# Optimization experiments

Hardware: AMD Instinct MI355X
Metric: run time of the kernel (lower is better)

Reference implementation:

```python
import jax, jax.numpy as jnp
import numpy as np

N_NODES = 50000
K_EIG = 512
F_DIM = 128


def setup_inputs() -> dict:
    key = jax.random.key(0)
    k1, k2, k3 = jax.random.split(key, 3)
    eigenvectors = jax.random.normal(k1, (N_NODES, K_EIG), dtype=jnp.float32)
    spectral_filters = jax.random.normal(k2, (K_EIG,), dtype=jnp.float32)
    x = jax.random.normal(k3, (N_NODES, F_DIM), dtype=jnp.float32)
    return {"eigenvectors": eigenvectors, "spectral_filters": spectral_filters, "x": x}


def reference(eigenvectors, spectral_filters, x):
    # U @ diag(g) @ U.T @ x  ==  U @ (g[:, None] * (U.T @ x)); relu epilogue.
    spec = eigenvectors.T @ x                      # [k, f]
    logits = eigenvectors @ (spectral_filters[:, None] * spec)  # [n, f]
    return jax.nn.relu(logits)
```

## Files before the change

### kernel.cpp

```cpp
#include <hip/hip_runtime.h>
#include <hip/hip_bf16.h>

#define N_NODES 50000
#define K_EIG   512
#define F_DIM   128
#define NPAD    51200
#define NSPLITS 160
#define CHUNK   320
#define NT32    1600
#define NT16    3200

typedef __attribute__((ext_vector_type(8))) short bf16x8;
typedef __attribute__((ext_vector_type(4))) short s16x4;
typedef __attribute__((ext_vector_type(4))) float f32x4;
typedef __attribute__((ext_vector_type(2))) unsigned u32x2;

static __device__ __forceinline__ unsigned pk2(float lo, float hi) {
    unsigned short a = __builtin_bit_cast(unsigned short, __float2bfloat16(lo));
    unsigned short b = __builtin_bit_cast(unsigned short, __float2bfloat16(hi));
    return ((unsigned)b << 16) | (unsigned)a;
}

static __device__ __forceinline__ short f2bf(float f) {
    union { float f; unsigned u; } v; v.f = f;
    unsigned r = v.u + 0x7fffu + ((v.u >> 16) & 1u);
    return (short)(r >> 16);
}

static __device__ __forceinline__ float bf2f(unsigned short u) {
    union { unsigned u; float f; } v; v.u = ((unsigned)u) << 16;
    return v.f;
}

__global__ __launch_bounds__(256) void prep_x(const float* __restrict__ x,
                                              unsigned short* __restrict__ xTa)
{
    const int n0 = blockIdx.x * 64;
    const int f0 = blockIdx.y * 64;
    const int fa = threadIdx.x & 15;
    const int nb = threadIdx.x >> 4;
    const int n  = n0 + 4 * nb;
    const int f  = f0 + 4 * fa;

    float r[4][4];
    #pragma unroll
    for (int jj = 0; jj < 4; ++jj) {
        int nr = n + jj;
        if (nr < N_NODES) {
            f32x4 v = *reinterpret_cast<const f32x4*>(x + (long)nr * F_DIM + f);
            r[jj][0] = v[0]; r[jj][1] = v[1]; r[jj][2] = v[2]; r[jj][3] = v[3];
        } else {
            r[jj][0] = r[jj][1] = r[jj][2] = r[jj][3] = 0.f;
        }
    }
    const int nt32 = n >> 5;
    const int hpart = ((n >> 3) & 3) * 16;
    const int slot  = 4 * (nb & 1);
    #pragma unroll
    for (int i = 0; i < 4; ++i) {
        int fi = f + i;
        size_t ad = ((size_t)((fi >> 4) * NT32 + nt32) * 64 + hpart + (fi & 15)) * 8 + slot;
        u32x2 w; w[0] = pk2(r[0][i], r[1][i]); w[1] = pk2(r[2][i], r[3][i]);
        *reinterpret_cast<u32x2*>(xTa + ad) = w;
    }
}

__global__ __launch_bounds__(256) void prep_u(const float* __restrict__ U,
                                              unsigned short* __restrict__ UTa,
                                              unsigned short* __restrict__ Ubfa)
{
    __shared__ unsigned char lds1[64 * 128];
    __shared__ unsigned char lds2[64 * 128];

    const int n0  = blockIdx.x * 64;
    const int k0  = blockIdx.y * 64;
    const int tid = threadIdx.x;
    const int kq  = tid & 15;
    const int nq  = tid >> 4;

    float r[4][4];
    #pragma unroll
    for (int j = 0; j < 4; ++j) {
        int n = n0 + 4 * nq + j;
        if (n < N_NODES) {
            f32x4 v = *reinterpret_cast<const f32x4*>(U + (long)n * K_EIG + k0 + 4 * kq);
            r[j][0] = v[0]; r[j][1] = v[1]; r[j][2] = v[2]; r[j][3] = v[3];
        } else {
            r[j][0] = r[j][1] = r[j][2] = r[j][3] = 0.f;
        }
    }

    #pragma unroll
    for (int i = 0; i < 4; ++i) {
        int kl = 4 * kq + i;
        unsigned lo = pk2(r[0][i], r[1][i]);
        unsigned hi = pk2(r[2][i], r[3][i]);
        int byte = (kl * 128 + 8 * nq) ^ ((kl & 7) << 4);
        *reinterpret_cast<unsigned long long*>(lds1 + byte) =
            ((unsigned long long)hi << 32) | (unsigned long long)lo;
    }
    #pragma unroll
    for (int j = 0; j < 4; ++j) {
        int nl = 4 * nq + j;
        unsigned lo = pk2(r[j][0], r[j][1]);
        unsigned hi = pk2(r[j][2], r[j][3]);
        int byte = (nl * 128 + 8 * kq) ^ ((nl & 7) << 4);
        *reinterpret_cast<unsigned long long*>(lds2 + byte) =
            ((unsigned long long)hi << 32) | (unsigned long long)lo;
    }
    __syncthreads();

    const int q = tid & 31;
    {
        const int fid = tid >> 5;
        const int ntl = fid >> 1;
        const int ktl = fid & 1;
        #pragma unroll
        for (int e = 0; e < 2; ++e) {
            int l    = 2 * q + e;
            int row  = ntl * 16 + (l & 15);
            int byte = (row * 128 + ktl * 64 + 16 * (l >> 4)) ^ ((row & 7) << 4);
            bf16x8 v = *reinterpret_cast<const bf16x8*>(lds2 + byte);
            size_t ad = (((size_t)(n0 >> 4) + ntl) * 16 + ((k0 >> 5) + ktl)) * 64 + l;
            *reinterpret_cast<bf16x8*>(Ubfa + ad * 8) = v;
        }
    }
    {
        const int fid = tid >> 5;
        const int ktl = fid >> 1;
        const int ntl = fid & 1;
        #pragma unroll
        for (int e = 0; e < 2; ++e) {
            int l    = 2 * q + e;
            int row  = ktl * 16 + (l & 15);
            int byte = (row * 128 + ntl * 64 + 16 * (l >> 4)) ^ ((row & 7) << 4);
            bf16x8 v = *reinterpret_cast<const bf16x8*>(lds1 + byte);
            size_t ad = (((size_t)(k0 >> 4) + ktl) * NT32 + ((n0 >> 5) + ntl)) * 64 + l;
            *reinterpret_cast<bf16x8*>(UTa + ad * 8) = v;
        }
    }
}

__global__ __launch_bounds__(256) void k_spec(
    const unsigned short* __restrict__ UTa, const unsigned short* __restrict__ xTa,
    unsigned short* __restrict__ part2)
{
    const int ktB   = blockIdx.x;
    const int split = blockIdx.y;
    const int tid   = threadIdx.x;
    const int wid   = tid >> 6;
    const int lane  = tid & 63;
    const int nt0   = split * (CHUNK / 32);

    f32x4 acc[4][2];
    #pragma unroll
    for (int s = 0; s < 4; ++s)
        #pragma unroll
        for (int t = 0; t < 2; ++t)
            #pragma unroll
            for (int e = 0; e < 4; ++e) acc[s][t][e] = 0.f;

    const unsigned short* Abase = UTa + ((size_t)(ktB * 4) * NT32) * 512 + lane * 8;
    const unsigned short* Bbase = xTa + ((size_t)(wid * 2) * NT32) * 512 + lane * 8;

    bf16x8 aC[4], bC[2];
    #pragma unroll
    for (int s = 0; s < 4; ++s)
        aC[s] = *reinterpret_cast<const bf16x8*>(Abase + ((size_t)s * NT32 + nt0) * 512);
    #pragma unroll
    for (int t = 0; t < 2; ++t)
        bC[t] = *reinterpret_cast<const bf16x8*>(Bbase + ((size_t)t * NT32 + nt0) * 512);

    for (int step = 0; step < CHUNK / 32; ++step) {
        int ntn = nt0 + ((step + 1 < CHUNK / 32) ? step + 1 : 0);
        bf16x8 aN[4], bN[2];
        #pragma unroll
        for (int s = 0; s < 4; ++s)
            aN[s] = *reinterpret_cast<const bf16x8*>(Abase + ((size_t)s * NT32 + ntn) * 512);
        #pragma unroll
        for (int t = 0; t < 2; ++t)
            bN[t] = *reinterpret_cast<const bf16x8*>(Bbase + ((size_t)t * NT32 + ntn) * 512);

        #pragma unroll
        for (int s = 0; s < 4; ++s)
            #pragma unroll
            for (int t = 0; t < 2; ++t)
                acc[s][t] = __builtin_amdgcn_mfma_f32_16x16x32_bf16(
                    aC[s], bC[t], acc[s][t], 0, 0, 0);

        #pragma unroll
        for (int s = 0; s < 4; ++s) aC[s] = aN[s];
        #pragma unroll
        for (int t = 0; t < 2; ++t) bC[t] = bN[t];
    }

    unsigned short* pb = part2 + (((size_t)(ktB * NSPLITS + split)) * 256 + tid) * 32;
    #pragma unroll
    for (int s = 0; s < 4; ++s) {
        bf16x8 v;
        #pragma unroll
        for (int e = 0; e < 4; ++e) {
            v[e]     = f2bf(acc[s][0][e]);
            v[e + 4] = f2bf(acc[s][1][e]);
        }
        *reinterpret_cast<bf16x8*>(pb + s * 8) = v;
    }
}

__global__ __launch_bounds__(256) void k_reduce1(
    const unsigned short* __restrict__ part2, float* __restrict__ part3)
{
    const int q  = blockIdx.x * 256 + threadIdx.x;
    const int pg = blockIdx.y;
    const int kt = q >> 11;
    const int tp = (q >> 3) & 255;
    const int sl = q & 7;
    f32x4 s; s[0] = s[1] = s[2] = s[3] = 0.f;
    const int pend = pg * 20 + 20;
    for (int p = pg * 20; p < pend; ++p) {
        s16x4 v = *reinterpret_cast<const s16x4*>(
            part2 + (((size_t)(kt * NSPLITS + p)) * 256 + tp) * 32 + sl * 4);
        s[0] += bf2f((unsigned short)v[0]); s[1] += bf2f((unsigned short)v[1]);
        s[2] += bf2f((unsigned short)v[2]); s[3] += bf2f((unsigned short)v[3]);
    }
    *reinterpret_cast<f32x4*>(part3 + ((size_t)pg * 16384 + q) * 4) = s;
}

__global__ __launch_bounds__(256) void k_reduce2(
    const float* __restrict__ part3, const float* __restrict__ g,
    unsigned short* __restrict__ specbfa)
{
    const int q = blockIdx.x * 256 + threadIdx.x;
    f32x4 s; s[0] = s[1] = s[2] = s[3] = 0.f;
    #pragma unroll
    for (int pg = 0; pg < 8; ++pg) {
        f32x4 v = *reinterpret_cast<const f32x4*>(part3 + ((size_t)pg * 16384 + q) * 4);
        s[0] += v[0]; s[1] += v[1]; s[2] += v[2]; s[3] += v[3];
    }
    const int kt = q >> 11, tp = (q >> 3) & 255, sl = q & 7;
    const int wid = tp >> 6, le = tp & 63, hh = le >> 4, mm = le & 15;
    const int ss = sl >> 1, tt = sl & 1;
    const int f = wid * 32 + tt * 16 + mm;
    const int k = kt * 64 + ss * 16 + hh * 4;
    f32x4 gv = *reinterpret_cast<const f32x4*>(g + k);
    s16x4 o;
    #pragma unroll
    for (int e = 0; e < 4; ++e) o[e] = f2bf(s[e] * gv[e]);
    const int lanep = ((k >> 3) & 3) * 16 + (f & 15);
    size_t ad = ((size_t)((f >> 4) * 16 + (k >> 5)) * 64 + lanep) * 8 + (k & 7);
    *reinterpret_cast<s16x4*>(specbfa + ad) = o;
}

__global__ __launch_bounds__(256) void k_out_bf(
    const unsigned short* __restrict__ Ubfa,
    const unsigned short* __restrict__ specbfa,
    float* __restrict__ out)
{
    const int tid  = threadIdx.x;
    const int wid  = tid >> 6;
    const int lane = tid & 63;
    const int h = lane >> 4, m = lane & 15;
    const int wr = wid >> 1, wc = wid & 1;
    const int nbase = blockIdx.x * 64 + wr * 32;
    const int fbase = wc * 64;

    const unsigned short* Al[2];
    #pragma unroll
    for (int i = 0; i < 2; ++i)
        Al[i] = Ubfa + ((size_t)((nbase >> 4) + i) * 8192 + lane * 8);
    const unsigned short* Blp[4];
    #pragma unroll
    for (int t = 0; t < 4; ++t)
        Blp[t] = specbfa + ((size_t)(4 * wc + t) * 8192 + lane * 8);

    f32x4 acc[2][4];
    #pragma unroll
    for (int i = 0; i < 2; ++i)
        #pragma unroll
        for (int t = 0; t < 4; ++t)
            #pragma unroll
            for (int e = 0; e < 4; ++e) acc[i][t][e] = 0.f;

    bf16x8 aC[2], bC[4];
    #pragma unroll
    for (int i = 0; i < 2; ++i) aC[i] = *reinterpret_cast<const bf16x8*>(Al[i]);
    #pragma unroll
    for (int t = 0; t < 4; ++t) bC[t] = *reinterpret_cast<const bf16x8*>(Blp[t]);

    for (int kb = 0; kb < 16; ++kb) {
        int kn = (kb + 1 < 16) ? kb + 1 : 0;
        bf16x8 aN[2], bN[4];
        #pragma unroll
        for (int i = 0; i < 2; ++i)
            aN[i] = *reinterpret_cast<const bf16x8*>(Al[i] + (size_t)kn * 512);
        #pragma unroll
        for (int t = 0; t < 4; ++t)
            bN[t] = *reinterpret_cast<const bf16x8*>(Blp[t] + (size_t)kn * 512);

        #pragma unroll
        for (int i = 0; i < 2; ++i)
            #pragma unroll
            for (int t = 0; t < 4; ++t)
                acc[i][t] = __builtin_amdgcn_mfma_f32_16x16x32_bf16(
                    aC[i], bC[t], acc[i][t], 0, 0, 0);

        #pragma unroll
        for (int i = 0; i < 2; ++i) aC[i] = aN[i];
        #pragma unroll
        for (int t = 0; t < 4; ++t) bC[t] = bN[t];
    }

    #pragma unroll
    for (int i = 0; i < 2; ++i)
        #pragma unroll
        for (int r = 0; r < 4; ++r) {
            int nn = nbase + 16 * i + 4 * h + r;
            if (nn < N_NODES) {
                float* orow = out + (long)nn * F_DIM + fbase + m;
                #pragma unroll
                for (int t = 0; t < 4; ++t)
                    orow[16 * t] = fmaxf(acc[i][t][r], 0.f);
            }
        }
}

__global__ __launch_bounds__(256) void k_spec_v1(
    const float* __restrict__ U, const float* __restrict__ g,
    const float* __restrict__ x, float* __restrict__ specT)
{
    const int kt    = blockIdx.x;
    const int split = blockIdx.y;
    const int tid   = threadIdx.x;
    const int wid   = tid >> 6;
    const int lane  = tid & 63;
    const int h     = lane >> 4;
    const int m     = lane & 15;
    const int k0 = kt * 64;
    const int f0 = wid * 32;
    const int chunk1 = 782;
    const int n_start = split * chunk1;
    int n_end = n_start + chunk1;
    if (n_end > N_NODES) n_end = N_NODES;

    f32x4 acc[4][2];
    #pragma unroll
    for (int s = 0; s < 4; ++s)
        #pragma unroll
        for (int t = 0; t < 2; ++t)
            #pragma unroll
            for (int e = 0; e < 4; ++e) acc[s][t][e] = 0.f;

    for (int nb = n_start; nb < n_end; nb += 32) {
        bf16x8 a[4]; bf16x8 b[2];
        const int nrow = nb + 8 * h;
        #pragma unroll
        for (int j = 0; j < 8; ++j) {
            int nn = nrow + j;
            bool valid = (nn < n_end);
            int nc = valid ? nn : (n_end - 1);
            const float* Urow = U + (long)nc * K_EIG + k0 + m;
            const float* Xrow = x + (long)nc * F_DIM + f0 + m;
            #pragma unroll
            for (int s = 0; s < 4; ++s) {
                short bv = f2bf(Urow[16 * s]);
                a[s][j] = valid ? bv : (short)0;
            }
            #pragma unroll
            for (int t = 0; t < 2; ++t) {
                short bv = f2bf(Xrow[16 * t]);
                b[t][j] = valid ? bv : (short)0;
            }
        }
        #pragma unroll
        for (int s = 0; s < 4; ++s)
            #pragma unroll
            for (int t = 0; t < 2; ++t)
                acc[s][t] = __builtin_amdgcn_mfma_f32_16x16x32_bf16(
                    a[s], b[t], acc[s][t], 0, 0, 0);
    }
    #pragma unroll
    for (int s = 0; s < 4; ++s)
        #pragma unroll
        for (int t = 0; t < 2; ++t)
            #pragma unroll
            for (int r = 0; r < 4; ++r) {
                int k = k0 + 16 * s + 4 * h + r;
                int f = f0 + 16 * t + m;
                atomicAdd(&specT[(long)f * K_EIG + k], acc[s][t][r] * g[k]);
            }
}

__global__ __launch_bounds__(256) void k_out_v1(
    const float* __restrict__ U, const float* __restrict__ specT,
    float* __restrict__ out)
{
    const int tid  = threadIdx.x;
    const int wid  = tid >> 6;
    const int lane = tid & 63;
    const int h = lane >> 4, m = lane & 15;
    const int wr = wid >> 1, wc = wid & 1;
    const int nbase = blockIdx.x * 128 + wr * 64;
    const int fbase = wc * 64;

    f32x4 acc[4][4];
    #pragma unroll
    for (int i = 0; i < 4; ++i)
        #pragma unroll
        for (int t = 0; t < 4; ++t)
            #pragma unroll
            for (int e = 0; e < 4; ++e) acc[i][t][e] = 0.f;

    for (int kb = 0; kb < K_EIG; kb += 32) {
        bf16x8 a[4], b[4];
        #pragma unroll
        for (int i = 0; i < 4; ++i) {
            int nn = nbase + 16 * i + m;
            bool valid = (nn < N_NODES);
            int nc = valid ? nn : (N_NODES - 1);
            const f32x4* p = reinterpret_cast<const f32x4*>(
                U + (long)nc * K_EIG + kb + 8 * h);
            f32x4 lo = p[0], hi = p[1];
            #pragma unroll
            for (int j = 0; j < 4; ++j) {
                short b0 = f2bf(lo[j]), b1 = f2bf(hi[j]);
                a[i][j]     = valid ? b0 : (short)0;
                a[i][j + 4] = valid ? b1 : (short)0;
            }
        }
        #pragma unroll
        for (int t = 0; t < 4; ++t) {
            const f32x4* p = reinterpret_cast<const f32x4*>(
                specT + (long)(fbase + 16 * t + m) * K_EIG + kb + 8 * h);
            f32x4 lo = p[0], hi = p[1];
            #pragma unroll
            for (int j = 0; j < 4; ++j) {
                b[t][j]     = f2bf(lo[j]);
                b[t][j + 4] = f2bf(hi[j]);
            }
        }
        #pragma unroll
        for (int i = 0; i < 4; ++i)
            #pragma unroll
            for (int t = 0; t < 4; ++t)
                acc[i][t] = __builtin_amdgcn_mfma_f32_16x16x32_bf16(
                    a[i], b[t], acc[i][t], 0, 0, 0);
    }
    #pragma unroll
    for (int i = 0; i < 4; ++i)
        #pragma unroll
        for (int r = 0; r < 4; ++r) {
            int nn = nbase + 16 * i + 4 * h + r;
            if (nn < N_NODES) {
                float* orow = out + (long)nn * F_DIM + fbase + m;
                #pragma unroll
                for (int t = 0; t < 4; ++t)
                    orow[16 * t] = fmaxf(acc[i][t][r], 0.f);
            }
        }
}

extern "C" void kernel_launch(void* const* d_in, const int* in_sizes, int n_in,
                              void* d_out, int out_size, void* d_ws, size_t ws_size,
                              hipStream_t stream) {
    const float* U = (const float*)d_in[0];
    const float* g = (const float*)d_in[1];
    const float* x = (const float*)d_in[2];
    float* out = (float*)d_out;

    const size_t OFF_XTA   = 0;
    const size_t OFF_UTA   = 13107200;
    const size_t OFF_UBFA  = 65536000;
    const size_t OFF_PART2 = 117964800;
    const size_t OFF_PART3 = 138936320;
    const size_t OFF_SPECA = 141033472;
    const size_t WS_NEEDED = 141164544;

    if (ws_size >= WS_NEEDED) {
        unsigned short* xTa     = (unsigned short*)((char*)d_ws + OFF_XTA);
        unsigned short* UTa     = (unsigned short*)((char*)d_ws + OFF_UTA);
        unsigned short* Ubfa    = (unsigned short*)((char*)d_ws + OFF_UBFA);
        unsigned short* part2   = (unsigned short*)((char*)d_ws + OFF_PART2);
        float*          part3   = (float*)((char*)d_ws + OFF_PART3);
        unsigned short* specbfa = (unsigned short*)((char*)d_ws + OFF_SPECA);

        dim3 gx(NPAD / 64, F_DIM / 64);
        prep_x<<<gx, 256, 0, stream>>>(x, xTa);

        dim3 gu(NPAD / 64, K_EIG / 64);
        prep_u<<<gu, 256, 0, stream>>>(U, UTa, Ubfa);

        dim3 g1(K_EIG / 64, NSPLITS);
        k_spec<<<g1, 256, 0, stream>>>(UTa, xTa, part2);

        dim3 gr1(64, 8);
        k_reduce1<<<gr1, 256, 0, stream>>>(part2, part3);
        k_reduce2<<<64, 256, 0, stream>>>(part3, g, specbfa);

        int nb2 = (N_NODES + 63) / 64;
        k_out_bf<<<nb2, 256, 0, stream>>>(Ubfa, specbfa, out);
    } else {
        float* specT = (float*)d_ws;
        hipMemsetAsync(specT, 0, (size_t)K_EIG * F_DIM * sizeof(float), stream);
        dim3 g1(K_EIG / 64, 64);
        k_spec_v1<<<g1, 256, 0, stream>>>(U, g, x, specT);
        int nb2 = (N_NODES + 127) / 128;
        k_out_v1<<<nb2, 256, 0, stream>>>(U, specT, out);
    }
}
```

Measured before the change: 107.1 us.

## Process four node tiles per prep_u block with register prefetch and double-buffered LDS

The prep_u conversion kernel now handles four consecutive 64-node tiles per block instead of one, shrinking the grid fourfold. While the current tile is packed and transposed through LDS, it loads the next tile's fp32 values into registers, and it alternates between two LDS buffers so only one barrier per tile is needed. The aim is to hide global load latency and cut block launch overhead in this bandwidth-bound prep step. The cost is more registers and LDS per block and less parallelism across the grid.

```diff
diff --git a/kernel.cpp b/kernel.cpp
--- a/kernel.cpp
+++ b/kernel.cpp
@@ -69,19 +69,25 @@
                                               unsigned short* __restrict__ UTa,
                                               unsigned short* __restrict__ Ubfa)
 {
-    __shared__ unsigned char lds1[64 * 128];
-    __shared__ unsigned char lds2[64 * 128];
-
-    const int n0  = blockIdx.x * 64;
+    __shared__ unsigned char lds1[2][64 * 128];
+    __shared__ unsigned char lds2[2][64 * 128];
+
+    const int ng  = blockIdx.x * 256;
     const int k0  = blockIdx.y * 64;
     const int tid = threadIdx.x;
     const int kq  = tid & 15;
     const int nq  = tid >> 4;
 
-    float r[4][4];
+    const int fid = tid >> 5;
+    const int q   = tid & 31;
+    const int ntlU = fid >> 1, ktlU = fid & 1;
+    const int ktlT = fid >> 1, ntlT = fid & 1;
+
+    float r[4][4], rN[4][4];
+
     #pragma unroll
     for (int j = 0; j < 4; ++j) {
-        int n = n0 + 4 * nq + j;
+        int n = ng + 4 * nq + j;
         if (n < N_NODES) {
             f32x4 v = *reinterpret_cast<const f32x4*>(U + (long)n * K_EIG + k0 + 4 * kq);
             r[j][0] = v[0]; r[j][1] = v[1]; r[j][2] = v[2]; r[j][3] = v[3];
@@ -91,52 +97,68 @@
     }
 
     #pragma unroll
-    for (int i = 0; i < 4; ++i) {
-        int kl = 4 * kq + i;
-        unsigned lo = pk2(r[0][i], r[1][i]);
-        unsigned hi = pk2(r[2][i], r[3][i]);
-        int byte = (kl * 128 + 8 * nq) ^ ((kl & 7) << 4);
-        *reinterpret_cast<unsigned long long*>(lds1 + byte) =
-            ((unsigned long long)hi << 32) | (unsigned long long)lo;
-    }
-    #pragma unroll
-    for (int j = 0; j < 4; ++j) {
-        int nl = 4 * nq + j;
-        unsigned lo = pk2(r[j][0], r[j][1]);
-        unsigned hi = pk2(r[j][2], r[j][3]);
-        int byte = (nl * 128 + 8 * kq) ^ ((nl & 7) << 4);
-        *reinterpret_cast<unsigned long long*>(lds2 + byte) =
-            ((unsigned long long)hi << 32) | (unsigned long long)lo;
-    }
-    __syncthreads();
-
-    const int q = tid & 31;
-    {
-        const int fid = tid >> 5;
-        const int ntl = fid >> 1;
-        const int ktl = fid & 1;
+    for (int s = 0; s < 4; ++s) {
+        const int n0  = ng + s * 64;
+        const int buf = s & 1;
+
+        if (s < 3) {
+            #pragma unroll
+            for (int j = 0; j < 4; ++j) {
+                int n = n0 + 64 + 4 * nq + j;
+                if (n < N_NODES) {
+                    f32x4 v = *reinterpret_cast<const f32x4*>(
+                        U + (long)n * K_EIG + k0 + 4 * kq);
+                    rN[j][0] = v[0]; rN[j][1] = v[1]; rN[j][2] = v[2]; rN[j][3] = v[3];
+                } else {
+                    rN[j][0] = rN[j][1] = rN[j][2] = rN[j][3] = 0.f;
+                }
+            }
+        }
+
+        #pragma unroll
+        for (int i = 0; i < 4; ++i) {
+            int kl = 4 * kq + i;
+            unsigned lo = pk2(r[0][i], r[1][i]);
+            unsigned hi = pk2(r[2][i], r[3][i]);
+            int byte = (kl * 128 + 8 * nq) ^ ((kl & 7) << 4);
+            *reinterpret_cast<unsigned long long*>(&lds1[buf][byte]) =
+                ((unsigned long long)hi << 32) | (unsigned long long)lo;
+        }
+        #pragma unroll
+        for (int j = 0; j < 4; ++j) {
+            int nl = 4 * nq + j;
+            unsigned lo = pk2(r[j][0], r[j][1]);
+            unsigned hi = pk2(r[j][2], r[j][3]);
+            int byte = (nl * 128 + 8 * kq) ^ ((nl & 7) << 4);
+            *reinterpret_cast<unsigned long long*>(&lds2[buf][byte]) =
+                ((unsigned long long)hi << 32) | (unsigned long long)lo;
+        }
+        __syncthreads();
+
         #pragma unroll
         for (int e = 0; e < 2; ++e) {
             int l    = 2 * q + e;
-            int row  = ntl * 16 + (l & 15);
-            int byte = (row * 128 + ktl * 64 + 16 * (l >> 4)) ^ ((row & 7) << 4);
-            bf16x8 v = *reinterpret_cast<const bf16x8*>(lds2 + byte);
-            size_t ad = (((size_t)(n0 >> 4) + ntl) * 16 + ((k0 >> 5) + ktl)) * 64 + l;
+            int row  = ntlU * 16 + (l & 15);
+            int byte = (row * 128 + ktlU * 64 + 16 * (l >> 4)) ^ ((row & 7) << 4);
+            bf16x8 v = *reinterpret_cast<const bf16x8*>(&lds2[buf][byte]);
+            size_t ad = (((size_t)(n0 >> 4) + ntlU) * 16 + ((k0 >> 5) + ktlU)) * 64 + l;
             *reinterpret_cast<bf16x8*>(Ubfa + ad * 8) = v;
         }
-    }
-    {
-        const int fid = tid >> 5;
-        const int ktl = fid >> 1;
-        const int ntl = fid & 1;
         #pragma unroll
         for (int e = 0; e < 2; ++e) {
             int l    = 2 * q + e;
-            int row  = ktl * 16 + (l & 15);
-            int byte = (row * 128 + ntl * 64 + 16 * (l >> 4)) ^ ((row & 7) << 4);
-            bf16x8 v = *reinterpret_cast<const bf16x8*>(lds1 + byte);
-            size_t ad = (((size_t)(k0 >> 4) + ktl) * NT32 + ((n0 >> 5) + ntl)) * 64 + l;
+            int row  = ktlT * 16 + (l & 15);
+            int byte = (row * 128 + ntlT * 64 + 16 * (l >> 4)) ^ ((row & 7) << 4);
+            bf16x8 v = *reinterpret_cast<const bf16x8*>(&lds1[buf][byte]);
+            size_t ad = (((size_t)(k0 >> 4) + ktlT) * NT32 + ((n0 >> 5) + ntlT)) * 64 + l;
             *reinterpret_cast<bf16x8*>(UTa + ad * 8) = v;
+        }
+
+        if (s < 3) {
+            #pragma unroll
+            for (int j = 0; j < 4; ++j)
+                #pragma unroll
+                for (int i = 0; i < 4; ++i) r[j][i] = rN[j][i];
         }
     }
 }
@@ -486,7 +508,7 @@
         dim3 gx(NPAD / 64, F_DIM / 64);
         prep_x<<<gx, 256, 0, stream>>>(x, xTa);
 
-        dim3 gu(NPAD / 64, K_EIG / 64);
+        dim3 gu(NPAD / 256, K_EIG / 64);
         prep_u<<<gu, 256, 0, stream>>>(U, UTa, Ubfa);
 
         dim3 g1(K_EIG / 64, NSPLITS);
```

Result: slower. 117.0 us (+9.2%).
